# Performance work log

Measured on AMD Instinct MI355X. Metric: run time of the kernel, lower is better.

## Reference

```python
import jax, jax.numpy as jnp
import numpy as np

B, S, D, H = 2, 2048, 1024, 16
DK = D // H  # 64


def setup_inputs() -> dict:
    key = jax.random.key(0)
    ks = jax.random.split(key, 11)
    std = 1.0 / np.sqrt(D)
    inp = {
        "q": jax.random.normal(ks[0], (B, S, D), jnp.float32),
        "k": jax.random.normal(ks[1], (B, S, D), jnp.float32),
        "v": jax.random.normal(ks[2], (B, S, D), jnp.float32),
        # causal mask: True means masked (matches masked_fill(mask == True, -1e9))
        "mask": jnp.triu(jnp.ones((1, 1, S, S), dtype=bool), k=1),
        "Wq": jax.random.normal(ks[3], (D, D), jnp.float32) * std,
        "bq": jnp.zeros((D,), jnp.float32),
        "Wk": jax.random.normal(ks[4], (D, D), jnp.float32) * std,
        "bk": jnp.zeros((D,), jnp.float32),
        "Wv": jax.random.normal(ks[5], (D, D), jnp.float32) * std,
        "bv": jnp.zeros((D,), jnp.float32),
        "Wo": jax.random.normal(ks[6], (D, D), jnp.float32) * std,
        "bo": jnp.zeros((D,), jnp.float32),
    }
    return inp


def _split_heads(x):
    b, s, _ = x.shape
    return x.reshape(b, s, H, DK).transpose(0, 2, 1, 3)  # [B,H,S,DK]


def reference(q, k, v, mask, Wq, bq, Wk, bk, Wv, bv, Wo, bo):
    # QKV projections (nn.Linear: x @ W.T + b)
    qh = _split_heads(q @ Wq.T + bq)
    kh = _split_heads(k @ Wk.T + bk)
    vh = _split_heads(v @ Wv.T + bv)
    # scaled dot-product attention (dropout is identity in eval)
    scores = jnp.einsum("bhqd,bhkd->bhqk", qh, kh) / jnp.sqrt(
        jnp.asarray(DK, jnp.float32))
    scores = jnp.where(mask, jnp.float32(-1e9), scores)
    attn = jax.nn.softmax(scores, axis=-1)
    out = jnp.einsum("bhqk,bhkd->bhqd", attn, vh)
    # combine heads [B,H,S,DK] -> [B,S,D], then output projection
    out = out.transpose(0, 2, 1, 3).reshape(q.shape[0], -1, D)
    return out @ Wo.T + bo
```

## Files before the change

kernel.cpp:

```cpp
#include <hip/hip_runtime.h>
#include <stdint.h>

#define S_LEN 2048
#define DMODEL 1024
#define NHEAD 16
#define DKH 64

typedef __attribute__((ext_vector_type(8))) short short8;
typedef __attribute__((ext_vector_type(4))) short sv4;
typedef __attribute__((ext_vector_type(4))) float fv4;
typedef __attribute__((ext_vector_type(8))) __bf16 bf16x8;
typedef __attribute__((ext_vector_type(4))) float f32x4;

#define QSCALE 0.18033688011112042f

static __device__ __forceinline__ short f2bf(float f) {
  unsigned u = __builtin_bit_cast(unsigned, f);
  u = u + 0x7fffu + ((u >> 16) & 1u);
  return (short)(u >> 16);
}

static __device__ __forceinline__ bf16x8 ldfrag(const void* p) {
  return __builtin_bit_cast(bf16x8, *(const short8*)p);
}

#define GLL16(gp, lp) __builtin_amdgcn_global_load_lds( \
    (const __attribute__((address_space(1))) unsigned int*)(const void*)(gp), \
    (__attribute__((address_space(3))) unsigned int*)(void*)(lp), 16, 0, 0)

#define WAIT_VMCNT0() asm volatile("s_waitcnt vmcnt(0)" ::: "memory")
#define WAIT_LGKM0()  asm volatile("s_waitcnt lgkmcnt(0)" ::: "memory")

__global__ __launch_bounds__(256) void convert_all(
    const float* __restrict__ q, const float* __restrict__ k, const float* __restrict__ v,
    const float* __restrict__ wq, const float* __restrict__ wk, const float* __restrict__ wv,
    const float* __restrict__ wo,
    short* __restrict__ xb, short* __restrict__ wb, short* __restrict__ wob)
{
  const int total = 4194304;
  for (int gid = blockIdx.x * blockDim.x + threadIdx.x; gid < total;
       gid += gridDim.x * blockDim.x) {
    const float* src; short* dst; int off; float scl = 1.0f;
    if (gid < 3145728) {
      int z = gid >> 20;
      off = (gid & 1048575) << 2;
      src = (z == 0) ? q : (z == 1) ? k : v;
      dst = xb + (size_t)z * 4194304;
    } else {
      int g = gid - 3145728;
      int z = g >> 18;
      off = (g & 262143) << 2;
      src = (z == 0) ? wq : (z == 1) ? wk : (z == 2) ? wv : wo;
      dst = (z < 3) ? (wb + (size_t)z * 1048576) : wob;
      if (z == 0) scl = QSCALE;
    }
    fv4 f = *(const fv4*)(src + off);
    sv4 o;
    o.x = f2bf(f.x * scl); o.y = f2bf(f.y * scl);
    o.z = f2bf(f.z * scl); o.w = f2bf(f.w * scl);
    *(sv4*)(dst + off) = o;
  }
}

__global__ __launch_bounds__(256) void gemm_bt(
    const short* __restrict__ Abase, const short* __restrict__ Wbase,
    const float* __restrict__ bias0, const float* __restrict__ bias1,
    const float* __restrict__ bias2, float bscl0,
    short* __restrict__ Cbf, float* __restrict__ Cf)
{
  const int Kd = 1024, Nd = 1024, Md = 4096;
  const int z = blockIdx.z;
  const short* A = Abase + (size_t)z * Md * Kd;
  const short* W = Wbase + (size_t)z * Nd * Kd;
  const float* bias = (z == 0) ? bias0 : (z == 1) ? bias1 : bias2;
  const float bscl = (z == 0) ? bscl0 : 1.0f;

  __shared__ short8 As[1024];
  __shared__ short8 Bs[1024];

  const int tid = threadIdx.x;
  const int w = tid >> 6, lane = tid & 63;
  const int wr = w >> 1, wc = w & 1;
  const int lhi = lane >> 4, llo = lane & 15;
  const int m0 = blockIdx.y * 128, n0 = blockIdx.x * 128;

  const f32x4 zero = {0.f, 0.f, 0.f, 0.f};
  f32x4 acc[4][4];
#pragma unroll
  for (int i = 0; i < 4; ++i)
#pragma unroll
    for (int j = 0; j < 4; ++j) acc[i][j] = zero;

  for (int kt = 0; kt < Kd / 64; ++kt) {
    const int k0 = kt * 64;
    __syncthreads();
#pragma unroll
    for (int inst = 0; inst < 4; ++inst) {
      int ib = w * 4096 + inst * 1024 + lane * 16;
      int row = ib >> 7;
      int colb = (ib & 127) ^ ((row & 7) << 4);
      int col = colb >> 1;
      GLL16(A + (size_t)(m0 + row) * Kd + k0 + col,
            (char*)As + (w * 4096 + inst * 1024));
      GLL16(W + (size_t)(n0 + row) * Kd + k0 + col,
            (char*)Bs + (w * 4096 + inst * 1024));
    }
    __syncthreads();
#pragma unroll
    for (int kk = 0; kk < 2; ++kk) {
      bf16x8 af[4], bfm[4];
#pragma unroll
      for (int t = 0; t < 4; ++t) {
        int arow = wr * 64 + t * 16 + llo;
        int abyte = ((arow << 7) + ((kk * 32 + lhi * 8) << 1)) ^ ((arow & 7) << 4);
        af[t] = ldfrag((const char*)As + abyte);
        int brow = wc * 64 + t * 16 + llo;
        int bbyte = ((brow << 7) + ((kk * 32 + lhi * 8) << 1)) ^ ((brow & 7) << 4);
        bfm[t] = ldfrag((const char*)Bs + bbyte);
      }
#pragma unroll
      for (int i = 0; i < 4; ++i)
#pragma unroll
        for (int j = 0; j < 4; ++j)
          acc[i][j] = __builtin_amdgcn_mfma_f32_16x16x32_bf16(af[i], bfm[j], acc[i][j], 0, 0, 0);
    }
  }

  short* Co = Cbf ? (Cbf + (size_t)z * Md * Nd) : nullptr;
#pragma unroll
  for (int i = 0; i < 4; ++i) {
#pragma unroll
    for (int j = 0; j < 4; ++j) {
#pragma unroll
      for (int r = 0; r < 4; ++r) {
        int row = m0 + wr * 64 + i * 16 + lhi * 4 + r;
        int col = n0 + wc * 64 + j * 16 + llo;
        float vv = acc[i][j][r] + bias[col] * bscl;
        if (Co) Co[(size_t)row * Nd + col] = f2bf(vv);
        else    Cf[(size_t)row * Nd + col] = vv;
      }
    }
  }
}

__global__ __launch_bounds__(256) void attn_fwd(
    const short* __restrict__ Qp, const short* __restrict__ Kp,
    const short* __restrict__ Vp, short* __restrict__ Out)
{
  __shared__ short8 Ks[2][512];
  __shared__ short  Vt[2][64 * 72];
  __shared__ short  PsA[4][16 * 72];

  const int tid = threadIdx.x;
  const int w = tid >> 6, lane = tid & 63;
  const int lhi = lane >> 4, llo = lane & 15;
  const int x = blockIdx.x;
  const int bh = blockIdx.y;
  const int b = bh >> 4, h = bh & 15;
  const size_t rowbase = (size_t)b * S_LEN;
  const short* Kbase = Kp + rowbase * DMODEL + h * DKH;
  const short* Vbase = Vp + rowbase * DMODEL + h * DKH;

  const int dg = tid & 15, kvg = tid >> 4;
  short* Ps = PsA[w];
  const f32x4 zero = {0.f, 0.f, 0.f, 0.f};

  for (int seq = 0; seq < 2; ++seq) {
    const int qt = (seq == 0) ? x : (31 - x);
    const int nt = qt + 1;
    const int qbase = qt * 64;

    __syncthreads();

    bf16x8 qf[2];
    {
      const short* qrow = Qp + (rowbase + qbase + w * 16 + llo) * DMODEL + h * DKH;
      qf[0] = ldfrag(qrow + lhi * 8);
      qf[1] = ldfrag(qrow + 32 + lhi * 8);
    }

    float mr[4], lr[4];
    f32x4 oacc[4];
#pragma unroll
    for (int r = 0; r < 4; ++r) { mr[r] = -3.0e38f; lr[r] = 0.f; }
#pragma unroll
    for (int dt = 0; dt < 4; ++dt) oacc[dt] = zero;

#pragma unroll
    for (int inst = 0; inst < 2; ++inst) {
      int ib = w * 2048 + inst * 1024 + lane * 16;
      int row = ib >> 7;
      int colb = (ib & 127) ^ ((row & 7) << 4);
      GLL16(Kbase + (size_t)row * DMODEL + (colb >> 1),
            (char*)&Ks[0][0] + (w * 2048 + inst * 1024));
    }
    sv4 vr0, vr1, vr2, vr3;
    vr0 = *(const sv4*)(Vbase + (size_t)(kvg * 4 + 0) * DMODEL + dg * 4);
    vr1 = *(const sv4*)(Vbase + (size_t)(kvg * 4 + 1) * DMODEL + dg * 4);
    vr2 = *(const sv4*)(Vbase + (size_t)(kvg * 4 + 2) * DMODEL + dg * 4);
    vr3 = *(const sv4*)(Vbase + (size_t)(kvg * 4 + 3) * DMODEL + dg * 4);

    for (int t = 0; t < nt; ++t) {
      const int cur = t & 1, nxt = cur ^ 1;
      const int kvbase = t * 64;

      WAIT_VMCNT0();
#pragma unroll
      for (int d = 0; d < 4; ++d) {
        sv4 wv;
        wv.x = vr0[d]; wv.y = vr1[d]; wv.z = vr2[d]; wv.w = vr3[d];
        *(sv4*)&Vt[cur][(dg * 4 + d) * 72 + kvg * 4] = wv;
      }
      if (t + 1 < nt) {
        const int nb = kvbase + 64;
#pragma unroll
        for (int inst = 0; inst < 2; ++inst) {
          int ib = w * 2048 + inst * 1024 + lane * 16;
          int row = ib >> 7;
          int colb = (ib & 127) ^ ((row & 7) << 4);
          GLL16(Kbase + (size_t)(nb + row) * DMODEL + (colb >> 1),
                (char*)&Ks[nxt][0] + (w * 2048 + inst * 1024));
        }
        vr0 = *(const sv4*)(Vbase + (size_t)(nb + kvg * 4 + 0) * DMODEL + dg * 4);
        vr1 = *(const sv4*)(Vbase + (size_t)(nb + kvg * 4 + 1) * DMODEL + dg * 4);
        vr2 = *(const sv4*)(Vbase + (size_t)(nb + kvg * 4 + 2) * DMODEL + dg * 4);
        vr3 = *(const sv4*)(Vbase + (size_t)(nb + kvg * 4 + 3) * DMODEL + dg * 4);
      }
      WAIT_LGKM0();
      __builtin_amdgcn_s_barrier();

      f32x4 sc[4];
#pragma unroll
      for (int tt = 0; tt < 4; ++tt) sc[tt] = zero;
      __builtin_amdgcn_s_setprio(1);
#pragma unroll
      for (int kk = 0; kk < 2; ++kk) {
#pragma unroll
        for (int tt = 0; tt < 4; ++tt) {
          int krow = tt * 16 + llo;
          int kbyte = ((krow << 7) + ((kk * 32 + lhi * 8) << 1)) ^ ((krow & 7) << 4);
          bf16x8 kf = ldfrag((const char*)&Ks[cur][0] + kbyte);
          sc[tt] = __builtin_amdgcn_mfma_f32_16x16x32_bf16(qf[kk], kf, sc[tt], 0, 0, 0);
        }
      }
      __builtin_amdgcn_s_setprio(0);

      const bool diag = (t == qt);
      float p[4][4];
#pragma unroll
      for (int r = 0; r < 4; ++r) {
        float tm = -3.0e38f;
#pragma unroll
        for (int tt = 0; tt < 4; ++tt) {
          float s = sc[tt][r];
          if (diag) {
            int kg = kvbase + tt * 16 + llo;
            int qg = qbase + w * 16 + lhi * 4 + r;
            if (kg > qg) s = -3.0e38f;
          }
          p[tt][r] = s;
          tm = fmaxf(tm, s);
        }
        tm = fmaxf(tm, __shfl_xor(tm, 1));
        tm = fmaxf(tm, __shfl_xor(tm, 2));
        tm = fmaxf(tm, __shfl_xor(tm, 4));
        tm = fmaxf(tm, __shfl_xor(tm, 8));
        float mnew = fmaxf(mr[r], tm);
        float alpha = __builtin_amdgcn_exp2f(mr[r] - mnew);
        mr[r] = mnew;
        float rs = 0.f;
#pragma unroll
        for (int tt = 0; tt < 4; ++tt) {
          float pv = __builtin_amdgcn_exp2f(p[tt][r] - mnew);
          p[tt][r] = pv;
          rs += pv;
        }
        rs += __shfl_xor(rs, 1);
        rs += __shfl_xor(rs, 2);
        rs += __shfl_xor(rs, 4);
        rs += __shfl_xor(rs, 8);
        lr[r] = lr[r] * alpha + rs;
#pragma unroll
        for (int dt = 0; dt < 4; ++dt) oacc[dt][r] = oacc[dt][r] * alpha;
#pragma unroll
        for (int tt = 0; tt < 4; ++tt)
          Ps[(lhi * 4 + r) * 72 + tt * 16 + llo] = f2bf(p[tt][r]);
      }

      __builtin_amdgcn_s_setprio(1);
#pragma unroll
      for (int kk = 0; kk < 2; ++kk) {
        bf16x8 pa = ldfrag(Ps + llo * 72 + kk * 32 + lhi * 8);
#pragma unroll
        for (int dt = 0; dt < 4; ++dt) {
          bf16x8 vf = ldfrag(&Vt[cur][(dt * 16 + llo) * 72 + kk * 32 + lhi * 8]);
          oacc[dt] = __builtin_amdgcn_mfma_f32_16x16x32_bf16(pa, vf, oacc[dt], 0, 0, 0);
        }
      }
      __builtin_amdgcn_s_setprio(0);
      __builtin_amdgcn_s_barrier();
    }

#pragma unroll
    for (int dt = 0; dt < 4; ++dt) {
#pragma unroll
      for (int r = 0; r < 4; ++r) {
        float vv = oacc[dt][r] / lr[r];
        int row = qbase + w * 16 + lhi * 4 + r;
        int col = h * DKH + dt * 16 + llo;
        Out[(rowbase + row) * DMODEL + col] = f2bf(vv);
      }
    }
  }
}

extern "C" void kernel_launch(void* const* d_in, const int* in_sizes, int n_in,
                              void* d_out, int out_size, void* d_ws, size_t ws_size,
                              hipStream_t stream) {
  (void)in_sizes; (void)n_in; (void)out_size; (void)ws_size;
  const float* q  = (const float*)d_in[0];
  const float* k  = (const float*)d_in[1];
  const float* v  = (const float*)d_in[2];
  const float* Wq = (const float*)d_in[4];
  const float* bq = (const float*)d_in[5];
  const float* Wk = (const float*)d_in[6];
  const float* bk = (const float*)d_in[7];
  const float* Wv = (const float*)d_in[8];
  const float* bv = (const float*)d_in[9];
  const float* Wo = (const float*)d_in[10];
  const float* bo = (const float*)d_in[11];
  float* out = (float*)d_out;

  short* xb   = (short*)d_ws;
  short* wb   = xb + 3ull * 4194304;
  short* wob  = wb + 3ull * 1048576;
  short* proj = wob + 1048576;
  short* attno = xb;

  convert_all<<<dim3(2048), dim3(256), 0, stream>>>(q, k, v, Wq, Wk, Wv, Wo, xb, wb, wob);
  gemm_bt<<<dim3(8, 32, 3), dim3(256), 0, stream>>>(xb, wb, bq, bk, bv, QSCALE, proj, nullptr);
  attn_fwd<<<dim3(16, 32), dim3(256), 0, stream>>>(proj, proj + 4194304ull,
                                                   proj + 2ull * 4194304, attno);
  gemm_bt<<<dim3(8, 32, 1), dim3(256), 0, stream>>>(attno, wob, bo, bo, bo, 1.0f, nullptr, out);
}
```

Before: 281.1 us.

## One query tile per block, lazy softmax rescale, and wider V transpose loads

The attention kernel no longer pairs two causal query tiles per block. It launches one block per query tile, heaviest first, doubling the grid so the scheduler can balance load. It adds a lazy online-softmax rescale: the running max and the output/denominator rescaling are updated only when some row's new max exceeds the old by more than a threshold, which skips exp and multiply work on most tiles. V staging now uses 16-byte row loads with scalar transposed LDS stores, which may raise LDS store count and bank conflicts.

```diff
diff --git a/kernel.cpp b/kernel.cpp
--- a/kernel.cpp
+++ b/kernel.cpp
@@ -154,162 +154,160 @@
   const int tid = threadIdx.x;
   const int w = tid >> 6, lane = tid & 63;
   const int lhi = lane >> 4, llo = lane & 15;
-  const int x = blockIdx.x;
+  const int qt = 31 - blockIdx.x;
+  const int nt = qt + 1;
+  const int qbase = qt * 64;
   const int bh = blockIdx.y;
   const int b = bh >> 4, h = bh & 15;
   const size_t rowbase = (size_t)b * S_LEN;
   const short* Kbase = Kp + rowbase * DMODEL + h * DKH;
   const short* Vbase = Vp + rowbase * DMODEL + h * DKH;
 
-  const int dg = tid & 15, kvg = tid >> 4;
   short* Ps = PsA[w];
   const f32x4 zero = {0.f, 0.f, 0.f, 0.f};
 
-  for (int seq = 0; seq < 2; ++seq) {
-    const int qt = (seq == 0) ? x : (31 - x);
-    const int nt = qt + 1;
-    const int qbase = qt * 64;
-
-    __syncthreads();
-
-    bf16x8 qf[2];
-    {
-      const short* qrow = Qp + (rowbase + qbase + w * 16 + llo) * DMODEL + h * DKH;
-      qf[0] = ldfrag(qrow + lhi * 8);
-      qf[1] = ldfrag(qrow + 32 + lhi * 8);
-    }
-
-    float mr[4], lr[4];
-    f32x4 oacc[4];
-#pragma unroll
-    for (int r = 0; r < 4; ++r) { mr[r] = -3.0e38f; lr[r] = 0.f; }
-#pragma unroll
-    for (int dt = 0; dt < 4; ++dt) oacc[dt] = zero;
-
-#pragma unroll
-    for (int inst = 0; inst < 2; ++inst) {
-      int ib = w * 2048 + inst * 1024 + lane * 16;
-      int row = ib >> 7;
-      int colb = (ib & 127) ^ ((row & 7) << 4);
-      GLL16(Kbase + (size_t)row * DMODEL + (colb >> 1),
-            (char*)&Ks[0][0] + (w * 2048 + inst * 1024));
-    }
-    sv4 vr0, vr1, vr2, vr3;
-    vr0 = *(const sv4*)(Vbase + (size_t)(kvg * 4 + 0) * DMODEL + dg * 4);
-    vr1 = *(const sv4*)(Vbase + (size_t)(kvg * 4 + 1) * DMODEL + dg * 4);
-    vr2 = *(const sv4*)(Vbase + (size_t)(kvg * 4 + 2) * DMODEL + dg * 4);
-    vr3 = *(const sv4*)(Vbase + (size_t)(kvg * 4 + 3) * DMODEL + dg * 4);
-
-    for (int t = 0; t < nt; ++t) {
-      const int cur = t & 1, nxt = cur ^ 1;
-      const int kvbase = t * 64;
-
-      WAIT_VMCNT0();
-#pragma unroll
-      for (int d = 0; d < 4; ++d) {
-        sv4 wv;
-        wv.x = vr0[d]; wv.y = vr1[d]; wv.z = vr2[d]; wv.w = vr3[d];
-        *(sv4*)&Vt[cur][(dg * 4 + d) * 72 + kvg * 4] = wv;
-      }
-      if (t + 1 < nt) {
-        const int nb = kvbase + 64;
-#pragma unroll
-        for (int inst = 0; inst < 2; ++inst) {
-          int ib = w * 2048 + inst * 1024 + lane * 16;
-          int row = ib >> 7;
-          int colb = (ib & 127) ^ ((row & 7) << 4);
-          GLL16(Kbase + (size_t)(nb + row) * DMODEL + (colb >> 1),
-                (char*)&Ks[nxt][0] + (w * 2048 + inst * 1024));
+  bf16x8 qf[2];
+  {
+    const short* qrow = Qp + (rowbase + qbase + w * 16 + llo) * DMODEL + h * DKH;
+    qf[0] = ldfrag(qrow + lhi * 8);
+    qf[1] = ldfrag(qrow + 32 + lhi * 8);
+  }
+
+  float mr[4], lr[4];
+  f32x4 oacc[4];
+#pragma unroll
+  for (int r = 0; r < 4; ++r) { mr[r] = -3.0e38f; lr[r] = 0.f; }
+#pragma unroll
+  for (int dt = 0; dt < 4; ++dt) oacc[dt] = zero;
+
+  const int kvs = lane, dgrp = w;
+
+#pragma unroll
+  for (int inst = 0; inst < 2; ++inst) {
+    int ib = w * 2048 + inst * 1024 + lane * 16;
+    int row = ib >> 7;
+    int colb = (ib & 127) ^ ((row & 7) << 4);
+    GLL16(Kbase + (size_t)row * DMODEL + (colb >> 1),
+          (char*)&Ks[0][0] + (w * 2048 + inst * 1024));
+  }
+  short8 va, vb;
+  va = *(const short8*)(Vbase + (size_t)kvs * DMODEL + dgrp * 16);
+  vb = *(const short8*)(Vbase + (size_t)kvs * DMODEL + dgrp * 16 + 8);
+
+  for (int t = 0; t < nt; ++t) {
+    const int cur = t & 1, nxt = cur ^ 1;
+    const int kvbase = t * 64;
+
+    WAIT_VMCNT0();
+#pragma unroll
+    for (int j = 0; j < 8; ++j) Vt[cur][(dgrp * 16 + j) * 72 + kvs] = va[j];
+#pragma unroll
+    for (int j = 0; j < 8; ++j) Vt[cur][(dgrp * 16 + 8 + j) * 72 + kvs] = vb[j];
+    if (t + 1 < nt) {
+      const int nb = kvbase + 64;
+#pragma unroll
+      for (int inst = 0; inst < 2; ++inst) {
+        int ib = w * 2048 + inst * 1024 + lane * 16;
+        int row = ib >> 7;
+        int colb = (ib & 127) ^ ((row & 7) << 4);
+        GLL16(Kbase + (size_t)(nb + row) * DMODEL + (colb >> 1),
+              (char*)&Ks[nxt][0] + (w * 2048 + inst * 1024));
+      }
+      va = *(const short8*)(Vbase + (size_t)(nb + kvs) * DMODEL + dgrp * 16);
+      vb = *(const short8*)(Vbase + (size_t)(nb + kvs) * DMODEL + dgrp * 16 + 8);
+    }
+    WAIT_LGKM0();
+    __builtin_amdgcn_s_barrier();
+
+    f32x4 sc[4];
+#pragma unroll
+    for (int tt = 0; tt < 4; ++tt) sc[tt] = zero;
+    __builtin_amdgcn_s_setprio(1);
+#pragma unroll
+    for (int kk = 0; kk < 2; ++kk) {
+#pragma unroll
+      for (int tt = 0; tt < 4; ++tt) {
+        int krow = tt * 16 + llo;
+        int kbyte = ((krow << 7) + ((kk * 32 + lhi * 8) << 1)) ^ ((krow & 7) << 4);
+        bf16x8 kf = ldfrag((const char*)&Ks[cur][0] + kbyte);
+        sc[tt] = __builtin_amdgcn_mfma_f32_16x16x32_bf16(qf[kk], kf, sc[tt], 0, 0, 0);
+      }
+    }
+    __builtin_amdgcn_s_setprio(0);
+
+    const bool diag = (t == qt);
+    float sv[4][4], tmx[4];
+#pragma unroll
+    for (int r = 0; r < 4; ++r) {
+      float trm = -3.0e38f;
+#pragma unroll
+      for (int tt = 0; tt < 4; ++tt) {
+        float s = sc[tt][r];
+        if (diag) {
+          int kg = kvbase + tt * 16 + llo;
+          int qg = qbase + w * 16 + lhi * 4 + r;
+          if (kg > qg) s = -3.0e38f;
         }
-        vr0 = *(const sv4*)(Vbase + (size_t)(nb + kvg * 4 + 0) * DMODEL + dg * 4);
-        vr1 = *(const sv4*)(Vbase + (size_t)(nb + kvg * 4 + 1) * DMODEL + dg * 4);
-        vr2 = *(const sv4*)(Vbase + (size_t)(nb + kvg * 4 + 2) * DMODEL + dg * 4);
-        vr3 = *(const sv4*)(Vbase + (size_t)(nb + kvg * 4 + 3) * DMODEL + dg * 4);
-      }
-      WAIT_LGKM0();
-      __builtin_amdgcn_s_barrier();
-
-      f32x4 sc[4];
-#pragma unroll
-      for (int tt = 0; tt < 4; ++tt) sc[tt] = zero;
-      __builtin_amdgcn_s_setprio(1);
-#pragma unroll
-      for (int kk = 0; kk < 2; ++kk) {
-#pragma unroll
-        for (int tt = 0; tt < 4; ++tt) {
-          int krow = tt * 16 + llo;
-          int kbyte = ((krow << 7) + ((kk * 32 + lhi * 8) << 1)) ^ ((krow & 7) << 4);
-          bf16x8 kf = ldfrag((const char*)&Ks[cur][0] + kbyte);
-          sc[tt] = __builtin_amdgcn_mfma_f32_16x16x32_bf16(qf[kk], kf, sc[tt], 0, 0, 0);
-        }
-      }
-      __builtin_amdgcn_s_setprio(0);
-
-      const bool diag = (t == qt);
-      float p[4][4];
+        sv[tt][r] = s;
+        trm = fmaxf(trm, s);
+      }
+      trm = fmaxf(trm, __shfl_xor(trm, 1));
+      trm = fmaxf(trm, __shfl_xor(trm, 2));
+      trm = fmaxf(trm, __shfl_xor(trm, 4));
+      trm = fmaxf(trm, __shfl_xor(trm, 8));
+      tmx[r] = trm;
+    }
+    bool grow = (tmx[0] > mr[0] + 8.f) || (tmx[1] > mr[1] + 8.f) ||
+                (tmx[2] > mr[2] + 8.f) || (tmx[3] > mr[3] + 8.f);
+    if (__ballot(grow)) {
 #pragma unroll
       for (int r = 0; r < 4; ++r) {
-        float tm = -3.0e38f;
-#pragma unroll
-        for (int tt = 0; tt < 4; ++tt) {
-          float s = sc[tt][r];
-          if (diag) {
-            int kg = kvbase + tt * 16 + llo;
-            int qg = qbase + w * 16 + lhi * 4 + r;
-            if (kg > qg) s = -3.0e38f;
-          }
-          p[tt][r] = s;
-          tm = fmaxf(tm, s);
-        }
-        tm = fmaxf(tm, __shfl_xor(tm, 1));
-        tm = fmaxf(tm, __shfl_xor(tm, 2));
-        tm = fmaxf(tm, __shfl_xor(tm, 4));
-        tm = fmaxf(tm, __shfl_xor(tm, 8));
-        float mnew = fmaxf(mr[r], tm);
+        float mnew = fmaxf(mr[r], tmx[r]);
         float alpha = __builtin_amdgcn_exp2f(mr[r] - mnew);
         mr[r] = mnew;
-        float rs = 0.f;
-#pragma unroll
-        for (int tt = 0; tt < 4; ++tt) {
-          float pv = __builtin_amdgcn_exp2f(p[tt][r] - mnew);
-          p[tt][r] = pv;
-          rs += pv;
-        }
-        rs += __shfl_xor(rs, 1);
-        rs += __shfl_xor(rs, 2);
-        rs += __shfl_xor(rs, 4);
-        rs += __shfl_xor(rs, 8);
-        lr[r] = lr[r] * alpha + rs;
+        lr[r] *= alpha;
 #pragma unroll
         for (int dt = 0; dt < 4; ++dt) oacc[dt][r] = oacc[dt][r] * alpha;
-#pragma unroll
-        for (int tt = 0; tt < 4; ++tt)
-          Ps[(lhi * 4 + r) * 72 + tt * 16 + llo] = f2bf(p[tt][r]);
-      }
-
-      __builtin_amdgcn_s_setprio(1);
-#pragma unroll
-      for (int kk = 0; kk < 2; ++kk) {
-        bf16x8 pa = ldfrag(Ps + llo * 72 + kk * 32 + lhi * 8);
-#pragma unroll
-        for (int dt = 0; dt < 4; ++dt) {
-          bf16x8 vf = ldfrag(&Vt[cur][(dt * 16 + llo) * 72 + kk * 32 + lhi * 8]);
-          oacc[dt] = __builtin_amdgcn_mfma_f32_16x16x32_bf16(pa, vf, oacc[dt], 0, 0, 0);
-        }
-      }
-      __builtin_amdgcn_s_setprio(0);
-      __builtin_amdgcn_s_barrier();
-    }
-
-#pragma unroll
-    for (int dt = 0; dt < 4; ++dt) {
-#pragma unroll
-      for (int r = 0; r < 4; ++r) {
-        float vv = oacc[dt][r] / lr[r];
-        int row = qbase + w * 16 + lhi * 4 + r;
-        int col = h * DKH + dt * 16 + llo;
-        Out[(rowbase + row) * DMODEL + col] = f2bf(vv);
-      }
+      }
+    }
+#pragma unroll
+    for (int r = 0; r < 4; ++r) {
+      float rs = 0.f;
+#pragma unroll
+      for (int tt = 0; tt < 4; ++tt) {
+        float pv = __builtin_amdgcn_exp2f(sv[tt][r] - mr[r]);
+        rs += pv;
+        Ps[(lhi * 4 + r) * 72 + tt * 16 + llo] = f2bf(pv);
+      }
+      rs += __shfl_xor(rs, 1);
+      rs += __shfl_xor(rs, 2);
+      rs += __shfl_xor(rs, 4);
+      rs += __shfl_xor(rs, 8);
+      lr[r] += rs;
+    }
+
+    __builtin_amdgcn_s_setprio(1);
+#pragma unroll
+    for (int kk = 0; kk < 2; ++kk) {
+      bf16x8 pa = ldfrag(Ps + llo * 72 + kk * 32 + lhi * 8);
+#pragma unroll
+      for (int dt = 0; dt < 4; ++dt) {
+        bf16x8 vf = ldfrag(&Vt[cur][(dt * 16 + llo) * 72 + kk * 32 + lhi * 8]);
+        oacc[dt] = __builtin_amdgcn_mfma_f32_16x16x32_bf16(pa, vf, oacc[dt], 0, 0, 0);
+      }
+    }
+    __builtin_amdgcn_s_setprio(0);
+    __builtin_amdgcn_s_barrier();
+  }
+
+#pragma unroll
+  for (int dt = 0; dt < 4; ++dt) {
+#pragma unroll
+    for (int r = 0; r < 4; ++r) {
+      float vv = oacc[dt][r] / lr[r];
+      int row = qbase + w * 16 + lhi * 4 + r;
+      int col = h * DKH + dt * 16 + llo;
+      Out[(rowbase + row) * DMODEL + col] = f2bf(vv);
     }
   }
 }
@@ -339,7 +337,7 @@
 
   convert_all<<<dim3(2048), dim3(256), 0, stream>>>(q, k, v, Wq, Wk, Wv, Wo, xb, wb, wob);
   gemm_bt<<<dim3(8, 32, 3), dim3(256), 0, stream>>>(xb, wb, bq, bk, bv, QSCALE, proj, nullptr);
-  attn_fwd<<<dim3(16, 32), dim3(256), 0, stream>>>(proj, proj + 4194304ull,
+  attn_fwd<<<dim3(32, 32), dim3(256), 0, stream>>>(proj, proj + 4194304ull,
                                                    proj + 2ull * 4194304, attno);
   gemm_bt<<<dim3(8, 32, 1), dim3(256), 0, stream>>>(attno, wob, bo, bo, bo, 1.0f, nullptr, out);
 }
```

Result: slower. 339.7 us (+20.8%).
